# Performance work log

Measured on AMD Instinct MI355X. Metric: run time of the kernel, lower is better.

## Reference

```python
import jax, jax.numpy as jnp
import numpy as np

N = 100000
E = 1600000
NFEAT, NHID, NCLASS = 128, 64, 40
EPS = 1e-5


def _sage_conv(x, src, dst, wl, wr, b):
    # mean aggregation over in-neighbors: out[dst] = mean_{src->dst} x[src]
    msg = jax.ops.segment_sum(x[src], dst, num_segments=N)          # [N, d]
    deg = jax.ops.segment_sum(jnp.ones((src.shape[0],), x.dtype), dst, num_segments=N)
    agg = msg / jnp.maximum(deg, 1.0)[:, None]
    return agg @ wl + x @ wr + b


def _bn_eval(x, g, b, m, v):
    return (x - m) * (g * jax.lax.rsqrt(v + EPS)) + b


def setup_inputs() -> dict:
    key = jax.random.key(0)
    ks = jax.random.split(key, 12)
    s = 0.05
    x = jax.random.normal(ks[0], (N, NFEAT), dtype=jnp.float32)
    edge_index = jax.random.randint(ks[1], (2, E), 0, N, dtype=jnp.int64)
    inp = {
        'x': x,
        'edge_index': edge_index,
        'w1l': jax.random.normal(ks[2], (NFEAT, NHID), jnp.float32) * s,
        'w1r': jax.random.normal(ks[3], (NFEAT, NHID), jnp.float32) * s,
        'b1': jnp.zeros((NHID,), jnp.float32),
        'wxl': jax.random.normal(ks[4], (NHID, NHID), jnp.float32) * s,
        'wxr': jax.random.normal(ks[5], (NHID, NHID), jnp.float32) * s,
        'bx': jnp.zeros((NHID,), jnp.float32),
        'w2l': jax.random.normal(ks[6], (NHID, NCLASS), jnp.float32) * s,
        'w2r': jax.random.normal(ks[7], (NHID, NCLASS), jnp.float32) * s,
        'b2': jnp.zeros((NCLASS,), jnp.float32),
        'bn3_g': jnp.ones((NHID,), jnp.float32),
        'bn3_b': jnp.zeros((NHID,), jnp.float32),
        'bn3_m': jax.random.normal(ks[8], (NHID,), jnp.float32) * 0.1,
        'bn3_v': jax.random.uniform(ks[9], (NHID,), jnp.float32, 0.5, 1.5),
        'bn2_g': jnp.ones((NCLASS,), jnp.float32),
        'bn2_b': jnp.zeros((NCLASS,), jnp.float32),
        'bn2_m': jax.random.normal(ks[10], (NCLASS,), jnp.float32) * 0.1,
        'bn2_v': jax.random.uniform(ks[11], (NCLASS,), jnp.float32, 0.5, 1.5),
    }
    return inp


def reference(x, edge_index, w1l, w1r, b1, wxl, wxr, bx, w2l, w2r, b2,
              bn3_g, bn3_b, bn3_m, bn3_v, bn2_g, bn2_b, bn2_m, bn2_v):
    src, dst = edge_index[0], edge_index[1]
    h = jax.nn.relu(_sage_conv(x, src, dst, w1l, w1r, b1))          # conv1 + relu
    # middle layer (layer=3 -> one convx iteration); dropout = identity (eval)
    h = _sage_conv(h, src, dst, wxl, wxr, bx)
    h = jax.nn.relu(_bn_eval(h, bn3_g, bn3_b, bn3_m, bn3_v))
    # final layer
    h = _sage_conv(h, src, dst, w2l, w2r, b2)
    return _bn_eval(h, bn2_g, bn2_b, bn2_m, bn2_v)                  # [N, NCLASS]
```

## Files before the change

kernel.cpp:

```cpp
#include <hip/hip_runtime.h>

#define NNODES 100000
#define NEDGES 1600000
#define NBK    196
#define BK_CAP 9000
#define CHUNK  4096

typedef short bhalf8 __attribute__((ext_vector_type(8)));
typedef float f32x4 __attribute__((ext_vector_type(4)));

__device__ __forceinline__ unsigned fbits(float x){ union{float f;unsigned u;}c; c.f=x; return c.u; }
__device__ __forceinline__ float bcast(unsigned u){ union{float f;unsigned u;}c; c.u=u; return c.f; }
__device__ __forceinline__ unsigned short rtn16(float x){
    unsigned u = fbits(x);
    return (unsigned short)((u + 0x7FFFu + ((u >> 16) & 1u)) >> 16);
}
__device__ __forceinline__ float b2f(unsigned short b){ return bcast((unsigned)b << 16); }

__global__ void detect_kernel(const int* __restrict__ ei, int* __restrict__ flag) {
    int t = threadIdx.x;
    int v = ei[2 * t + 1];
    unsigned long long nz = __ballot(v != 0);
    if (t == 0) flag[0] = (nz == 0ULL) ? 1 : 0;
}

__global__ __launch_bounds__(256) void bucketize(
    const int* __restrict__ ei, const int* __restrict__ flag,
    unsigned* __restrict__ recs, int* __restrict__ bcur) {
    const int is64 = flag[0];
    __shared__ int cnt[256], base[256], loc[256], rnk[256];
    __shared__ unsigned stage[CHUNK];
    __shared__ unsigned char bkof[CHUNK];
    const int t = threadIdx.x;
    const long start = (long)blockIdx.x * CHUNK;
    cnt[t] = 0; rnk[t] = 0;
    __syncthreads();
#pragma unroll
    for (int k = 0; k < CHUNK / 256; ++k) {
        long e = start + k * 256 + t;
        if (e < NEDGES) {
            int d = is64 ? ei[2 * (NEDGES + e)] : ei[NEDGES + e];
            atomicAdd(&cnt[d >> 9], 1);
        }
    }
    __syncthreads();
    int v = cnt[t];
    int run = v;
    loc[t] = run;
    __syncthreads();
    for (int off = 1; off < 256; off <<= 1) {
        int other = (t >= off) ? loc[t - off] : 0;
        __syncthreads();
        run += other;
        loc[t] = run;
        __syncthreads();
    }
    int excl = run - v;
    if (v > 0) base[t] = atomicAdd(&bcur[t], v);
    loc[t] = excl;
    __syncthreads();
#pragma unroll
    for (int k = 0; k < CHUNK / 256; ++k) {
        long e = start + k * 256 + t;
        if (e < NEDGES) {
            int s = is64 ? ei[2 * e] : ei[e];
            int d = is64 ? ei[2 * (NEDGES + e)] : ei[NEDGES + e];
            int b = d >> 9;
            int r = atomicAdd(&rnk[b], 1);
            int pos = loc[b] + r;
            stage[pos] = ((unsigned)s << 9) | (unsigned)(d & 511);
            bkof[pos] = (unsigned char)b;
        }
    }
    __syncthreads();
    const int tot = (int)min((long)CHUNK, NEDGES - start);
    for (int i = t; i < tot; i += 256) {
        int b = bkof[i];
        int pos = base[b] + (i - loc[b]);
        if (pos < BK_CAP)
            recs[(size_t)b * BK_CAP + pos] = stage[i];
    }
}

__global__ __launch_bounds__(512) void csr_build(
    const unsigned* __restrict__ recs, const int* __restrict__ bcur,
    int* __restrict__ offs, int* __restrict__ csr) {
    const int b = blockIdx.x;
    const int t = threadIdx.x;
    const int lo = b << 9;
    __shared__ int sc[512];
    __shared__ int hist[512];
    __shared__ int loff[512];
    int bv = (t < NBK) ? bcur[t] : 0;
    int run = bv;
    sc[t] = run;
    __syncthreads();
    for (int off = 1; off < 512; off <<= 1) {
        int other = (t >= off) ? sc[t - off] : 0;
        __syncthreads();
        run += other;
        sc[t] = run;
        __syncthreads();
    }
    const int n = bcur[b];
    const int csr_base = sc[b] - n;
    const unsigned* P = recs + (size_t)b * BK_CAP;
    hist[t] = 0;
    __syncthreads();
    for (int i = t; i < n; i += 512)
        atomicAdd(&hist[P[i] & 511], 1);
    __syncthreads();
    int hv = hist[t];
    int hrun = hv;
    sc[t] = hrun;
    __syncthreads();
    for (int off = 1; off < 512; off <<= 1) {
        int other = (t >= off) ? sc[t - off] : 0;
        __syncthreads();
        hrun += other;
        sc[t] = hrun;
        __syncthreads();
    }
    int ex = hrun - hv;
    loff[t] = ex;
    int node = lo + t;
    if (node < NNODES) offs[node] = csr_base + ex;
    if (b == NBK - 1 && t == 0) offs[NNODES] = NEDGES;
    __syncthreads();
    hist[t] = loff[t];
    __syncthreads();
    for (int i = t; i < n; i += 512) {
        unsigned rec = P[i];
        int r = atomicAdd(&hist[rec & 511], 1);
        csr[csr_base + r] = (int)(rec >> 9);
    }
}

template <int K, int NL, int NTOT>
__global__ void prep_w(const float* __restrict__ wl, const float* __restrict__ wr,
                       unsigned short* __restrict__ Bh, unsigned short* __restrict__ Bl) {
    constexpr int NCT = NTOT / 16;
    constexpr int TOT = (K / 32) * NCT * 512;
    for (int idx = blockIdx.x * blockDim.x + threadIdx.x; idx < TOT;
         idx += gridDim.x * blockDim.x) {
        int e = idx & 7, l = (idx >> 3) & 63, rest = idx >> 9;
        int ct = rest % NCT, kc = rest / NCT;
        int k = kc * 32 + (l >> 4) * 8 + e;
        int j = ct * 16 + (l & 15);
        float v = (j < NL) ? wl[k * NL + j] : wr[k * NL + (j - NL)];
        unsigned short h = rtn16(v);
        float r1 = v - bcast((unsigned)h << 16);
        Bh[idx] = h;
        Bl[idx] = rtn16(r1);
    }
}

template <int K, int NL, int NTOT, bool ABF16>
__global__ __launch_bounds__(256) void gemm_mfma(
    const void* __restrict__ hvp, const unsigned short* __restrict__ Bh,
    const unsigned short* __restrict__ Bl, const float* __restrict__ bias,
    unsigned short* __restrict__ zl, unsigned short* __restrict__ zr, int nrows) {
    constexpr int NCT = NTOT / 16;
    constexpr int NKC = K / 32;
    int t = threadIdx.x;
    int l = t & 63, w = t >> 6;
    int rb = blockIdx.x * 64 + w * 16;
    int arow = rb + (l & 15);
    int kg = l >> 4;
    f32x4 acc[NCT];
#pragma unroll
    for (int ct = 0; ct < NCT; ++ct) acc[ct] = (f32x4){0.f, 0.f, 0.f, 0.f};
    const bool aok = (arow < nrows);
#pragma unroll
    for (int kc = 0; kc < NKC; ++kc) {
        bhalf8 ah = {0,0,0,0,0,0,0,0}, al = {0,0,0,0,0,0,0,0};
        if (ABF16) {
            const unsigned short* hr =
                (const unsigned short*)hvp + (long)arow * K + kg * 8;
            if (aok) ah = *(const bhalf8*)(hr + kc * 32);
        } else {
            const float* hr = (const float*)hvp + (long)arow * K + kg * 8;
            float4 a0 = make_float4(0.f, 0.f, 0.f, 0.f), a1 = a0;
            if (aok) {
                a0 = *(const float4*)(hr + kc * 32);
                a1 = *(const float4*)(hr + kc * 32 + 4);
            }
            float av[8] = {a0.x, a0.y, a0.z, a0.w, a1.x, a1.y, a1.z, a1.w};
#pragma unroll
            for (int e = 0; e < 8; ++e) {
                unsigned short hh = rtn16(av[e]);
                float r1 = av[e] - bcast((unsigned)hh << 16);
                ah[e] = (short)hh;
                al[e] = (short)rtn16(r1);
            }
        }
        const unsigned short* hp = Bh + (size_t)(kc * NCT) * 512 + l * 8;
        const unsigned short* lp = Bl + (size_t)(kc * NCT) * 512 + l * 8;
#pragma unroll
        for (int ct = 0; ct < NCT; ++ct) {
            bhalf8 bh = *(const bhalf8*)(hp + ct * 512);
            bhalf8 bl = *(const bhalf8*)(lp + ct * 512);
            acc[ct] = __builtin_amdgcn_mfma_f32_16x16x32_bf16(ah, bh, acc[ct], 0, 0, 0);
            acc[ct] = __builtin_amdgcn_mfma_f32_16x16x32_bf16(ah, bl, acc[ct], 0, 0, 0);
            if (!ABF16)
                acc[ct] = __builtin_amdgcn_mfma_f32_16x16x32_bf16(al, bh, acc[ct], 0, 0, 0);
        }
    }
    int orow0 = rb + kg * 4;
#pragma unroll
    for (int ct = 0; ct < NCT; ++ct) {
        int j = ct * 16 + (l & 15);
        bool isl = (j < NL);
        int cc = isl ? j : j - NL;
        float bj = isl ? 0.f : bias[cc];
        unsigned short* __restrict__ dp = isl ? zl : zr;
#pragma unroll
        for (int r = 0; r < 4; ++r) {
            int orow = orow0 + r;
            if (orow < nrows) dp[(long)orow * NL + cc] = rtn16(acc[ct][r] + bj);
        }
    }
}

template <int NOUT, int MODE, typename OUTT>
__global__ __launch_bounds__(256) void combine_kernel(
    const unsigned short* __restrict__ zl, const unsigned short* __restrict__ zr,
    const int* __restrict__ offs, const int* __restrict__ csr,
    const float* __restrict__ g, const float* __restrict__ bb,
    const float* __restrict__ m, const float* __restrict__ v,
    OUTT* __restrict__ out) {
    int wid  = (blockIdx.x * blockDim.x + threadIdx.x) >> 6;
    int lane = threadIdx.x & 63;
    if (wid >= NNODES) return;
    int q   = lane >> 5;
    int li2 = (lane & 31) * 2;
    const bool cok = (li2 < NOUT);
    float zr0 = 0.f, zr1 = 0.f;
    float g0 = 0.f, g1 = 0.f, bb0 = 0.f, bb1 = 0.f;
    float m0 = 0.f, m1 = 0.f, v0 = 0.f, v1 = 0.f;
    if (cok) {
        ushort2 zb = *(const ushort2*)&zr[(long)wid * NOUT + li2];
        zr0 = b2f(zb.x); zr1 = b2f(zb.y);
        if (MODE == 1 || MODE == 2) {
            float2 t2;
            t2 = *(const float2*)&g[li2];  g0 = t2.x;  g1 = t2.y;
            t2 = *(const float2*)&bb[li2]; bb0 = t2.x; bb1 = t2.y;
            t2 = *(const float2*)&m[li2];  m0 = t2.x;  m1 = t2.y;
            t2 = *(const float2*)&v[li2];  v0 = t2.x;  v1 = t2.y;
        }
    }
    int s0 = offs[wid], s1 = offs[wid + 1];
    float ax = 0.f, ay = 0.f;
    for (int base = s0; base < s1; base += 64) {
        int c = min(64, s1 - base);
        int cm1 = c - 1;
        int sv = (base + lane < s1) ? csr[base + lane] : 0;
        for (int p0 = 0; p0 < c; p0 += 16) {
            ushort2 hv[8];
#pragma unroll
            for (int j = 0; j < 8; ++j) {
                int eidx = p0 + 2 * j + q;
                int srow = __shfl(sv, min(eidx, cm1));
                ushort2 tv = make_ushort2(0, 0);
                if (eidx < c && cok)
                    tv = *(const ushort2*)&zl[(long)srow * NOUT + li2];
                hv[j] = tv;
            }
#pragma unroll
            for (int j = 0; j < 8; ++j) {
                ax += b2f(hv[j].x); ay += b2f(hv[j].y);
            }
        }
    }
    ax += __shfl_xor(ax, 32);
    ay += __shfl_xor(ay, 32);
    if (q != 0 || !cok) return;
    float invd = 1.f / fmaxf((float)(s1 - s0), 1.f);
    float r0 = ax * invd + zr0;
    float r1 = ay * invd + zr1;
    if (MODE == 1 || MODE == 2) {
        r0 = (r0 - m0) * (g0 * rsqrtf(v0 + 1e-5f)) + bb0;
        r1 = (r1 - m1) * (g1 * rsqrtf(v1 + 1e-5f)) + bb1;
    }
    if (MODE == 0 || MODE == 1) {
        r0 = fmaxf(r0, 0.f); r1 = fmaxf(r1, 0.f);
    }
    if constexpr (MODE == 2) {
        *(float2*)&out[(long)wid * NOUT + li2] = make_float2(r0, r1);
    } else {
        *(ushort2*)&out[(long)wid * NOUT + li2] = make_ushort2(rtn16(r0), rtn16(r1));
    }
}

extern "C" void kernel_launch(void* const* d_in, const int* in_sizes, int n_in,
                              void* d_out, int out_size, void* d_ws, size_t ws_size,
                              hipStream_t stream) {
    const float* x    = (const float*)d_in[0];
    const int*   ei   = (const int*)d_in[1];
    const float* w1l  = (const float*)d_in[2];
    const float* w1r  = (const float*)d_in[3];
    const float* b1   = (const float*)d_in[4];
    const float* wxl  = (const float*)d_in[5];
    const float* wxr  = (const float*)d_in[6];
    const float* bx   = (const float*)d_in[7];
    const float* w2l  = (const float*)d_in[8];
    const float* w2r  = (const float*)d_in[9];
    const float* b2   = (const float*)d_in[10];
    const float* bn3g = (const float*)d_in[11];
    const float* bn3b = (const float*)d_in[12];
    const float* bn3m = (const float*)d_in[13];
    const float* bn3v = (const float*)d_in[14];
    const float* bn2g = (const float*)d_in[15];
    const float* bn2b = (const float*)d_in[16];
    const float* bn2m = (const float*)d_in[17];
    const float* bn2v = (const float*)d_in[18];
    float* out = (float*)d_out;

    char* p = (char*)d_ws;
    auto alloc = [&](size_t bytes) -> void* {
        void* r = (void*)p;
        p += (bytes + 255) & ~(size_t)255;
        return r;
    };
    int*   flag   = (int*)alloc(4);
    int*   bcur   = (int*)alloc(NBK * 4);
    int*   offs   = (int*)alloc((size_t)(NNODES + 1) * 4);
    int*   csr    = (int*)alloc((size_t)NEDGES * 4);
    unsigned short* h16  = (unsigned short*)alloc((size_t)NNODES * 64 * 2);
    unsigned short* zl16 = (unsigned short*)alloc((size_t)NNODES * 64 * 2);
    unsigned short* zr16 = (unsigned short*)alloc((size_t)NNODES * 64 * 2);
    unsigned short* B1h = (unsigned short*)alloc(16384 * 2);
    unsigned short* B1l = (unsigned short*)alloc(16384 * 2);
    unsigned short* B2h = (unsigned short*)alloc(8192 * 2);
    unsigned short* B2l = (unsigned short*)alloc(8192 * 2);
    unsigned short* B3h = (unsigned short*)alloc(5120 * 2);
    unsigned short* B3l = (unsigned short*)alloc(5120 * 2);
    unsigned* recs = (unsigned*)h16;

    hipMemsetAsync(bcur, 0, NBK * 4, stream);
    detect_kernel<<<1, 64, 0, stream>>>(ei, flag);
    bucketize<<<(NEDGES + CHUNK - 1) / CHUNK, 256, 0, stream>>>(ei, flag, recs, bcur);
    prep_w<128, 64, 128><<<64, 256, 0, stream>>>(w1l, w1r, B1h, B1l);
    prep_w<64, 64, 128><<<32, 256, 0, stream>>>(wxl, wxr, B2h, B2l);
    prep_w<64, 40, 80><<<20, 256, 0, stream>>>(w2l, w2r, B3h, B3l);
    csr_build<<<NBK, 512, 0, stream>>>(recs, bcur, offs, csr);

    const int GB = (NNODES + 63) / 64;
    gemm_mfma<128, 64, 128, false><<<GB, 256, 0, stream>>>(x, B1h, B1l, b1, zl16, zr16, NNODES);
    combine_kernel<64, 0, unsigned short><<<25000, 256, 0, stream>>>(
        zl16, zr16, offs, csr, nullptr, nullptr, nullptr, nullptr, h16);
    gemm_mfma<64, 64, 128, true><<<GB, 256, 0, stream>>>(h16, B2h, B2l, bx, zl16, zr16, NNODES);
    combine_kernel<64, 1, unsigned short><<<25000, 256, 0, stream>>>(
        zl16, zr16, offs, csr, bn3g, bn3b, bn3m, bn3v, h16);
    gemm_mfma<64, 40, 80, true><<<GB, 256, 0, stream>>>(h16, B3h, B3l, b2, zl16, zr16, NNODES);
    combine_kernel<40, 2, float><<<25000, 256, 0, stream>>>(
        zl16, zr16, offs, csr, bn2g, bn2b, bn2m, bn2v, out);
}
```

Before: 238.2 us.

## Fold batchnorm into weights, pre-scale CSR byte offsets, add full-chunk gather path

The eval-mode batchnorm scale and shift are folded into the GEMM weights and a fused bias during weight prep, so the combine kernels only do mean, add and relu. CSR entries now hold byte offsets into a zl buffer with a fixed 128-byte row stride, which removes a multiply from every gather. The gather loop also gets a bounds-check-free fast path for full 16-edge chunks. Folding the scale into the weights before bf16 splitting slightly changes rounding, and zl now always uses a 64-wide stride even when the layer has 40 outputs.

```diff
diff --git a/kernel.cpp b/kernel.cpp
--- a/kernel.cpp
+++ b/kernel.cpp
@@ -132,22 +132,33 @@
     for (int i = t; i < n; i += 512) {
         unsigned rec = P[i];
         int r = atomicAdd(&hist[rec & 511], 1);
-        csr[csr_base + r] = (int)(rec >> 9);
+        csr[csr_base + r] = (int)(rec >> 9) * 128;
     }
 }
 
 template <int K, int NL, int NTOT>
 __global__ void prep_w(const float* __restrict__ wl, const float* __restrict__ wr,
-                       unsigned short* __restrict__ Bh, unsigned short* __restrict__ Bl) {
+                       const float* __restrict__ bias,
+                       const float* __restrict__ g, const float* __restrict__ bb,
+                       const float* __restrict__ m, const float* __restrict__ vv,
+                       unsigned short* __restrict__ Bh, unsigned short* __restrict__ Bl,
+                       float* __restrict__ bfix) {
     constexpr int NCT = NTOT / 16;
     constexpr int TOT = (K / 32) * NCT * 512;
-    for (int idx = blockIdx.x * blockDim.x + threadIdx.x; idx < TOT;
-         idx += gridDim.x * blockDim.x) {
+    int tid = blockIdx.x * blockDim.x + threadIdx.x;
+    if (tid < NL) {
+        float sc = g ? g[tid] * rsqrtf(vv[tid] + 1e-5f) : 1.f;
+        float sh = g ? (bb[tid] - m[tid] * sc) : 0.f;
+        bfix[tid] = bias[tid] * sc + sh;
+    }
+    for (int idx = tid; idx < TOT; idx += gridDim.x * blockDim.x) {
         int e = idx & 7, l = (idx >> 3) & 63, rest = idx >> 9;
         int ct = rest % NCT, kc = rest / NCT;
         int k = kc * 32 + (l >> 4) * 8 + e;
         int j = ct * 16 + (l & 15);
-        float v = (j < NL) ? wl[k * NL + j] : wr[k * NL + (j - NL)];
+        int jj = (j < NL) ? j : j - NL;
+        float sc = g ? g[jj] * rsqrtf(vv[jj] + 1e-5f) : 1.f;
+        float v = ((j < NL) ? wl[k * NL + j] : wr[k * NL + (j - NL)]) * sc;
         unsigned short h = rtn16(v);
         float r1 = v - bcast((unsigned)h << 16);
         Bh[idx] = h;
@@ -213,41 +224,35 @@
         bool isl = (j < NL);
         int cc = isl ? j : j - NL;
         float bj = isl ? 0.f : bias[cc];
-        unsigned short* __restrict__ dp = isl ? zl : zr;
 #pragma unroll
         for (int r = 0; r < 4; ++r) {
             int orow = orow0 + r;
-            if (orow < nrows) dp[(long)orow * NL + cc] = rtn16(acc[ct][r] + bj);
-        }
-    }
-}
-
-template <int NOUT, int MODE, typename OUTT>
+            if (orow < nrows) {
+                if (isl) zl[(long)orow * 64 + cc] = rtn16(acc[ct][r]);
+                else     zr[(long)orow * NL + cc] = rtn16(acc[ct][r] + bj);
+            }
+        }
+    }
+}
+
+template <int NOUT, bool RELU, typename OUTT>
 __global__ __launch_bounds__(256) void combine_kernel(
     const unsigned short* __restrict__ zl, const unsigned short* __restrict__ zr,
     const int* __restrict__ offs, const int* __restrict__ csr,
-    const float* __restrict__ g, const float* __restrict__ bb,
-    const float* __restrict__ m, const float* __restrict__ v,
     OUTT* __restrict__ out) {
     int wid  = (blockIdx.x * blockDim.x + threadIdx.x) >> 6;
     int lane = threadIdx.x & 63;
     if (wid >= NNODES) return;
-    int q   = lane >> 5;
-    int li2 = (lane & 31) * 2;
-    const bool cok = (li2 < NOUT);
+    int q    = lane >> 5;
+    int li2  = (lane & 31) * 2;
+    int lib  = li2 * 2;
+    constexpr bool FULL = (NOUT == 64);
+    const bool cok = FULL || (li2 < NOUT);
+    const char* zlb = (const char*)zl;
     float zr0 = 0.f, zr1 = 0.f;
-    float g0 = 0.f, g1 = 0.f, bb0 = 0.f, bb1 = 0.f;
-    float m0 = 0.f, m1 = 0.f, v0 = 0.f, v1 = 0.f;
     if (cok) {
-        ushort2 zb = *(const ushort2*)&zr[(long)wid * NOUT + li2];
-        zr0 = b2f(zb.x); zr1 = b2f(zb.y);
-        if (MODE == 1 || MODE == 2) {
-            float2 t2;
-            t2 = *(const float2*)&g[li2];  g0 = t2.x;  g1 = t2.y;
-            t2 = *(const float2*)&bb[li2]; bb0 = t2.x; bb1 = t2.y;
-            t2 = *(const float2*)&m[li2];  m0 = t2.x;  m1 = t2.y;
-            t2 = *(const float2*)&v[li2];  v0 = t2.x;  v1 = t2.y;
-        }
+        unsigned u = *(const unsigned*)&zr[(long)wid * NOUT + li2];
+        zr0 = bcast(u << 16); zr1 = bcast(u & 0xFFFF0000u);
     }
     int s0 = offs[wid], s1 = offs[wid + 1];
     float ax = 0.f, ay = 0.f;
@@ -256,19 +261,30 @@
         int cm1 = c - 1;
         int sv = (base + lane < s1) ? csr[base + lane] : 0;
         for (int p0 = 0; p0 < c; p0 += 16) {
-            ushort2 hv[8];
+            unsigned hv[8];
+            if (p0 + 16 <= c) {
+#pragma unroll
+                for (int j = 0; j < 8; ++j) {
+                    int soff = __shfl(sv, p0 + 2 * j + q);
+                    unsigned tv = 0;
+                    if (cok) tv = *(const unsigned*)(zlb + soff + lib);
+                    hv[j] = tv;
+                }
+            } else {
+#pragma unroll
+                for (int j = 0; j < 8; ++j) {
+                    int eidx = p0 + 2 * j + q;
+                    int soff = __shfl(sv, min(eidx, cm1));
+                    unsigned tv = 0;
+                    if (eidx < c && cok)
+                        tv = *(const unsigned*)(zlb + soff + lib);
+                    hv[j] = tv;
+                }
+            }
 #pragma unroll
             for (int j = 0; j < 8; ++j) {
-                int eidx = p0 + 2 * j + q;
-                int srow = __shfl(sv, min(eidx, cm1));
-                ushort2 tv = make_ushort2(0, 0);
-                if (eidx < c && cok)
-                    tv = *(const ushort2*)&zl[(long)srow * NOUT + li2];
-                hv[j] = tv;
-            }
-#pragma unroll
-            for (int j = 0; j < 8; ++j) {
-                ax += b2f(hv[j].x); ay += b2f(hv[j].y);
+                ax += bcast(hv[j] << 16);
+                ay += bcast(hv[j] & 0xFFFF0000u);
             }
         }
     }
@@ -278,14 +294,8 @@
     float invd = 1.f / fmaxf((float)(s1 - s0), 1.f);
     float r0 = ax * invd + zr0;
     float r1 = ay * invd + zr1;
-    if (MODE == 1 || MODE == 2) {
-        r0 = (r0 - m0) * (g0 * rsqrtf(v0 + 1e-5f)) + bb0;
-        r1 = (r1 - m1) * (g1 * rsqrtf(v1 + 1e-5f)) + bb1;
-    }
-    if (MODE == 0 || MODE == 1) {
-        r0 = fmaxf(r0, 0.f); r1 = fmaxf(r1, 0.f);
-    }
-    if constexpr (MODE == 2) {
+    if (RELU) { r0 = fmaxf(r0, 0.f); r1 = fmaxf(r1, 0.f); }
+    if constexpr (sizeof(OUTT) == 4) {
         *(float2*)&out[(long)wid * NOUT + li2] = make_float2(r0, r1);
     } else {
         *(ushort2*)&out[(long)wid * NOUT + li2] = make_ushort2(rtn16(r0), rtn16(r1));
@@ -335,24 +345,27 @@
     unsigned short* B2l = (unsigned short*)alloc(8192 * 2);
     unsigned short* B3h = (unsigned short*)alloc(5120 * 2);
     unsigned short* B3l = (unsigned short*)alloc(5120 * 2);
+    float* bfix1 = (float*)alloc(64 * 4);
+    float* bfix2 = (float*)alloc(64 * 4);
+    float* bfix3 = (float*)alloc(40 * 4);
     unsigned* recs = (unsigned*)h16;
 
     hipMemsetAsync(bcur, 0, NBK * 4, stream);
     detect_kernel<<<1, 64, 0, stream>>>(ei, flag);
     bucketize<<<(NEDGES + CHUNK - 1) / CHUNK, 256, 0, stream>>>(ei, flag, recs, bcur);
-    prep_w<128, 64, 128><<<64, 256, 0, stream>>>(w1l, w1r, B1h, B1l);
-    prep_w<64, 64, 128><<<32, 256, 0, stream>>>(wxl, wxr, B2h, B2l);
-    prep_w<64, 40, 80><<<20, 256, 0, stream>>>(w2l, w2r, B3h, B3l);
+    prep_w<128, 64, 128><<<64, 256, 0, stream>>>(w1l, w1r, b1, nullptr, nullptr, nullptr, nullptr, B1h, B1l, bfix1);
+    prep_w<64, 64, 128><<<32, 256, 0, stream>>>(wxl, wxr, bx, bn3g, bn3b, bn3m, bn3v, B2h, B2l, bfix2);
+    prep_w<64, 40, 80><<<20, 256, 0, stream>>>(w2l, w2r, b2, bn2g, bn2b, bn2m, bn2v, B3h, B3l, bfix3);
     csr_build<<<NBK, 512, 0, stream>>>(recs, bcur, offs, csr);
 
     const int GB = (NNODES + 63) / 64;
-    gemm_mfma<128, 64, 128, false><<<GB, 256, 0, stream>>>(x, B1h, B1l, b1, zl16, zr16, NNODES);
-    combine_kernel<64, 0, unsigned short><<<25000, 256, 0, stream>>>(
-        zl16, zr16, offs, csr, nullptr, nullptr, nullptr, nullptr, h16);
-    gemm_mfma<64, 64, 128, true><<<GB, 256, 0, stream>>>(h16, B2h, B2l, bx, zl16, zr16, NNODES);
-    combine_kernel<64, 1, unsigned short><<<25000, 256, 0, stream>>>(
-        zl16, zr16, offs, csr, bn3g, bn3b, bn3m, bn3v, h16);
-    gemm_mfma<64, 40, 80, true><<<GB, 256, 0, stream>>>(h16, B3h, B3l, b2, zl16, zr16, NNODES);
-    combine_kernel<40, 2, float><<<25000, 256, 0, stream>>>(
-        zl16, zr16, offs, csr, bn2g, bn2b, bn2m, bn2v, out);
-}
+    gemm_mfma<128, 64, 128, false><<<GB, 256, 0, stream>>>(x, B1h, B1l, bfix1, zl16, zr16, NNODES);
+    combine_kernel<64, true, unsigned short><<<25000, 256, 0, stream>>>(
+        zl16, zr16, offs, csr, h16);
+    gemm_mfma<64, 64, 128, true><<<GB, 256, 0, stream>>>(h16, B2h, B2l, bfix2, zl16, zr16, NNODES);
+    combine_kernel<64, true, unsigned short><<<25000, 256, 0, stream>>>(
+        zl16, zr16, offs, csr, h16);
+    gemm_mfma<64, 40, 80, true><<<GB, 256, 0, stream>>>(h16, B3h, B3l, bfix3, zl16, zr16, NNODES);
+    combine_kernel<40, false, float><<<25000, 256, 0, stream>>>(
+        zl16, zr16, offs, csr, out);
+}
```

New measurement: 226.7 us. 1.05x faster.
